# Kernel optimization log

Hardware: AMD Instinct MI355X
Metric: run time of the kernel (lower is better)

Reference implementation:

```python
import jax, jax.numpy as jnp
import numpy as np

B, S, D, E, H = 8, 1024, 1024, 8, 4096  # batch, seq, n_embd, num_experts, 4*n_embd


def setup_inputs() -> dict:
    key = jax.random.key(0)
    ks = jax.random.split(key, 8)
    sc = 0.02
    return {
        "x": jax.random.normal(ks[0], (B, S, D), jnp.float32),
        "noise": jax.random.normal(ks[1], (B, S, E), jnp.float32),
        "Wg": jax.random.normal(ks[2], (D, E), jnp.float32) * sc,
        "bg": jnp.zeros((E,), jnp.float32),
        "Wn": jax.random.normal(ks[3], (D, E), jnp.float32) * sc,
        "bn": jnp.zeros((E,), jnp.float32),
        "W1": jax.random.normal(ks[4], (E, D, H), jnp.float32) * sc,
        "b1": jnp.zeros((E, H), jnp.float32),
        "W2": jax.random.normal(ks[5], (E, H, D), jnp.float32) * sc,
        "b2": jnp.zeros((E, D), jnp.float32),
        "top_k": 2,
    }


def reference(x, noise, Wg, bg, Wn, bn, W1, b1, W2, b2, top_k):
    # --- NoisyTopkRouter ---
    logits = jnp.einsum("bsd,de->bse", x, Wg) + bg
    noise_logits = jnp.einsum("bsd,de->bse", x, Wn) + bn
    noisy = logits + noise * jax.nn.softplus(noise_logits)  # [B,S,E]
    _, idx = jax.lax.top_k(noisy, top_k)  # [B,S,K]
    in_topk = jax.nn.one_hot(idx, noisy.shape[-1], dtype=noisy.dtype).sum(-2) > 0
    sparse_logits = jnp.where(in_topk, noisy, -jnp.inf)
    gating = jax.nn.softmax(sparse_logits, axis=-1)  # zero outside top-k

    # --- dispatch/combine: gating is exactly zero for non-selected experts,
    # so per-expert masked gather + weighted scatter-add == gated dense sum ---
    g_e = jnp.moveaxis(gating, -1, 0)  # [E,B,S]

    def body(acc, params):
        W1e, b1e, W2e, b2e, ge = params
        h = jax.nn.relu(jnp.einsum("bsd,dh->bsh", x, W1e) + b1e)  # [B,S,H]
        y = (jnp.einsum("bsh,hd->bsd", h, W2e) + b2e) * ge[..., None]
        return acc + y, y

    final_output, expert_outputs = jax.lax.scan(
        body, jnp.zeros_like(x), (W1, b1, W2, b2, g_e)
    )
    # expert_outputs: [E,B,S,D], matching the per-expert weighted outputs list
    return final_output, expert_outputs, gating
```

## Files before the change

kernel.cpp:

```cpp
#include <hip/hip_runtime.h>
#include <hip/hip_bf16.h>
#include <stdint.h>

#define TKN   8192
#define DD    1024
#define EE    8
#define HH    4096
#define TOPK  2
#define NASG  (TKN * TOPK)
#define NSLOT 72

typedef unsigned short u16;
typedef __bf16 bf16x8 __attribute__((ext_vector_type(8)));
typedef float  f32x4  __attribute__((ext_vector_type(4)));

__device__ __forceinline__ u16 f2bf(float f) {
  __hip_bfloat16 h = __float2bfloat16(f);
  return __builtin_bit_cast(u16, h);
}
__device__ __forceinline__ float bf2f(u16 u) {
  uint32_t v = ((uint32_t)u) << 16;
  return __builtin_bit_cast(float, v);
}

__device__ __forceinline__ void glds16(const void* g, void* l) {
  __builtin_amdgcn_global_load_lds(
      (__attribute__((address_space(1))) void*)g,
      (__attribute__((address_space(3))) void*)l, 16, 0, 0);
}

#define FENCE() asm volatile("" ::: "memory")
#define BAR()   do { FENCE(); __builtin_amdgcn_s_barrier(); FENCE(); } while (0)
#define VMCNT8() asm volatile("s_waitcnt vmcnt(8)" ::: "memory")
#define VMCNT0() asm volatile("s_waitcnt vmcnt(0)" ::: "memory")

__global__ __launch_bounds__(256) void transpose_cvt_kernel(
    const float* __restrict__ src, u16* __restrict__ dst, int R, int C) {
  __shared__ float tile[64][33];
  int e = blockIdx.z;
  int c0 = blockIdx.x * 32, r0 = blockIdx.y * 64;
  int tx = threadIdx.x, ty = threadIdx.y;
  const float* s = src + (size_t)e * R * C;
  uint32_t* d32 = (uint32_t*)(dst + (size_t)e * R * C);
#pragma unroll
  for (int j = 0; j < 8; j++)
    tile[ty * 8 + j][tx] = s[(size_t)(r0 + ty * 8 + j) * C + c0 + tx];
  __syncthreads();
#pragma unroll
  for (int jj = 0; jj < 4; jj++) {
    int c = c0 + ty * 4 + jj;
    uint32_t lo = f2bf(tile[2 * tx][ty * 4 + jj]);
    uint32_t hi = f2bf(tile[2 * tx + 1][ty * 4 + jj]);
    d32[((size_t)c * R + r0) / 2 + tx] = lo | (hi << 16);
  }
}

__global__ __launch_bounds__(256) void router_kernel(
    const float* __restrict__ x, const float* __restrict__ noise,
    const float* __restrict__ Wg, const float* __restrict__ bg,
    const float* __restrict__ Wn, const float* __restrict__ bn,
    float* __restrict__ gating, u16* __restrict__ xb,
    int* __restrict__ sel_e, float* __restrict__ sel_g) {
  int t = blockIdx.x;
  int tid = threadIdx.x;
  float acc[16];
#pragma unroll
  for (int j = 0; j < 16; j++) acc[j] = 0.f;
  for (int i = tid; i < DD; i += 256) {
    float xv = x[(size_t)t * DD + i];
    xb[(size_t)t * DD + i] = f2bf(xv);
    const float4* g4 = (const float4*)(Wg + (size_t)i * EE);
    const float4* n4 = (const float4*)(Wn + (size_t)i * EE);
    float4 ga = g4[0], gb = g4[1];
    float4 na = n4[0], nb = n4[1];
    acc[0] += xv * ga.x;  acc[1] += xv * ga.y;  acc[2] += xv * ga.z;  acc[3] += xv * ga.w;
    acc[4] += xv * gb.x;  acc[5] += xv * gb.y;  acc[6] += xv * gb.z;  acc[7] += xv * gb.w;
    acc[8] += xv * na.x;  acc[9] += xv * na.y;  acc[10] += xv * na.z; acc[11] += xv * na.w;
    acc[12] += xv * nb.x; acc[13] += xv * nb.y; acc[14] += xv * nb.z; acc[15] += xv * nb.w;
  }
  __shared__ float red[4][16];
  int lane = tid & 63, wv = tid >> 6;
#pragma unroll
  for (int j = 0; j < 16; j++) {
    float v = acc[j];
    for (int o = 32; o > 0; o >>= 1) v += __shfl_down(v, o);
    acc[j] = v;
  }
  if (lane == 0) {
#pragma unroll
    for (int j = 0; j < 16; j++) red[wv][j] = acc[j];
  }
  __syncthreads();
  if (tid == 0) {
    float nz[EE];
#pragma unroll
    for (int e = 0; e < EE; e++) {
      float dg = red[0][e] + red[1][e] + red[2][e] + red[3][e] + bg[e];
      float dn = red[0][8 + e] + red[1][8 + e] + red[2][8 + e] + red[3][8 + e] + bn[e];
      float sp = fmaxf(dn, 0.f) + log1pf(expf(-fabsf(dn)));
      nz[e] = dg + noise[(size_t)t * EE + e] * sp;
    }
    int m1 = 0;
    for (int e = 1; e < EE; e++) if (nz[e] > nz[m1]) m1 = e;
    int m2 = (m1 == 0) ? 1 : 0;
    for (int e = 0; e < EE; e++) if (e != m1 && nz[e] > nz[m2]) m2 = e;
    float eb = expf(nz[m2] - nz[m1]);
    float den = 1.f + eb;
    float g1 = 1.f / den, g2 = eb / den;
    gating[(size_t)t * EE + m1] = g1;
    gating[(size_t)t * EE + m2] = g2;
    sel_e[t * 2] = m1; sel_e[t * 2 + 1] = m2;
    sel_g[t * 2] = g1; sel_g[t * 2 + 1] = g2;
  }
}

__global__ __launch_bounds__(256) void hist_scan_kernel(
    const int* __restrict__ sel_e, int* __restrict__ counts,
    int* __restrict__ offsets, int* __restrict__ cursors,
    int* __restrict__ slots) {
  __shared__ int hist[EE];
  int tid = threadIdx.x;
  if (tid < EE) hist[tid] = 0;
  __syncthreads();
  for (int i = tid; i < NASG; i += 256) atomicAdd(&hist[sel_e[i]], 1);
  __syncthreads();
  if (tid == 0) {
    int off = 0, ns = 0;
    for (int e = 0; e < EE; e++) {
      int c = hist[e];
      counts[e] = c; offsets[e] = off; cursors[e] = off; off += c;
      int nrt = (c + 255) >> 8;
      for (int rt = 0; rt < nrt; rt++) slots[ns++] = (e << 16) | rt;
    }
    for (; ns < NSLOT; ns++) slots[ns] = -1;
  }
}

__global__ __launch_bounds__(256) void build_lists_kernel(
    const int* __restrict__ sel_e, const float* __restrict__ sel_g,
    int* __restrict__ cursors, int* __restrict__ tok_list,
    float* __restrict__ gate_list, int* __restrict__ asg_of) {
  int t = blockIdx.x * 256 + threadIdx.x;
  int lane = threadIdx.x & 63;
#pragma unroll
  for (int k = 0; k < TOPK; k++) {
    int e = sel_e[t * 2 + k];
    float g = sel_g[t * 2 + k];
    for (int ee = 0; ee < EE; ee++) {
      unsigned long long m = __ballot(e == ee);
      if (m) {
        int leader = __ffsll(m) - 1;
        int base = 0;
        if (lane == leader) base = atomicAdd(&cursors[ee], __popcll(m));
        base = __shfl(base, leader);
        if (e == ee) {
          int slot = base + __popcll(m & ((1ull << lane) - 1ull));
          tok_list[slot] = t;
          gate_list[slot] = g;
          asg_of[t * 2 + k] = slot;
        }
      }
    }
  }
}

__global__ __launch_bounds__(256) void zerofill_kernel(
    const float* __restrict__ gating, float* __restrict__ expert_out) {
  int id = blockIdx.x;
  int e = id >> 13, t = id & (TKN - 1);
  if (gating[(size_t)t * EE + e] != 0.f) return;
  float4* p = (float4*)(expert_out + ((size_t)e * TKN + t) * DD);
  p[threadIdx.x] = (float4){0.f, 0.f, 0.f, 0.f};
}

__global__ __launch_bounds__(256) void combine_kernel(
    const float* __restrict__ expert_out, const int* __restrict__ sel_e,
    float* __restrict__ final_out) {
  int t = blockIdx.x;
  int e1 = sel_e[2 * t], e2 = sel_e[2 * t + 1];
  const float4* r1 = (const float4*)(expert_out + ((size_t)e1 * TKN + t) * DD);
  const float4* r2 = (const float4*)(expert_out + ((size_t)e2 * TKN + t) * DD);
  float4* o = (float4*)(final_out + (size_t)t * DD);
  int i = threadIdx.x;
  float4 a = r1[i], b = r2[i];
  o[i] = (float4){a.x + b.x, a.y + b.y, a.z + b.z, a.w + b.w};
}

__global__ __launch_bounds__(256) void merge_combine_kernel(
    const u16* __restrict__ part, const int* __restrict__ asg_of,
    const int* __restrict__ sel_e, const float* __restrict__ sel_g,
    const float* __restrict__ b2, float* __restrict__ expert_out,
    float* __restrict__ final_out) {
  int t = blockIdx.x;
  int i = threadIdx.x;
  int i1 = asg_of[2 * t], i2 = asg_of[2 * t + 1];
  int e1 = sel_e[2 * t], e2 = sel_e[2 * t + 1];
  float g1 = sel_g[2 * t], g2 = sel_g[2 * t + 1];
  float s1[4] = {0.f, 0.f, 0.f, 0.f}, s2[4] = {0.f, 0.f, 0.f, 0.f};
#pragma unroll
  for (int kq = 0; kq < 4; kq++) {
    ushort4 a = ((const ushort4*)(part + ((size_t)kq * NASG + i1) * DD))[i];
    ushort4 b = ((const ushort4*)(part + ((size_t)kq * NASG + i2) * DD))[i];
    s1[0] += bf2f(a.x); s1[1] += bf2f(a.y); s1[2] += bf2f(a.z); s1[3] += bf2f(a.w);
    s2[0] += bf2f(b.x); s2[1] += bf2f(b.y); s2[2] += bf2f(b.z); s2[3] += bf2f(b.w);
  }
  float4 bb1 = ((const float4*)(b2 + (size_t)e1 * DD))[i];
  float4 bb2 = ((const float4*)(b2 + (size_t)e2 * DD))[i];
  float4 y1 = {(s1[0] + bb1.x) * g1, (s1[1] + bb1.y) * g1,
               (s1[2] + bb1.z) * g1, (s1[3] + bb1.w) * g1};
  float4 y2 = {(s2[0] + bb2.x) * g2, (s2[1] + bb2.y) * g2,
               (s2[2] + bb2.z) * g2, (s2[3] + bb2.w) * g2};
  ((float4*)(expert_out + ((size_t)e1 * TKN + t) * DD))[i] = y1;
  ((float4*)(expert_out + ((size_t)e2 * TKN + t) * DD))[i] = y2;
  ((float4*)(final_out + (size_t)t * DD))[i] =
      (float4){y1.x + y2.x, y1.y + y2.y, y1.z + y2.z, y1.w + y2.w};
}

template<int KLOOP, int KSTRIDE, bool GATHER, int EPI, int LOGC>
__global__ __launch_bounds__(512, 2) void gemm8_kernel(
    const u16* __restrict__ A, const u16* __restrict__ Bm,
    const float* __restrict__ bias, const int* __restrict__ tok_list,
    const float* __restrict__ gate_list, const int* __restrict__ counts,
    const int* __restrict__ offsets, const int* __restrict__ slots,
    int Ncols, u16* __restrict__ OutBf, float* __restrict__ outF,
    u16* __restrict__ outP) {
  constexpr int NT = KLOOP / 64;
  int gid = blockIdx.x;
  int q = gid >> 3;
  constexpr int PERX = 9 << LOGC;
  int kq = q / PERX;
  int r0q = q - kq * PERX;
  int slot = (gid & 7) * 9 + (r0q >> LOGC);
  int ct = r0q & ((1 << LOGC) - 1);
  int packed = slots[slot];
  if (packed < 0) return;
  int e = packed >> 16;
  int rt = packed & 0xffff;
  int cnt = counts[e];
  int off = offsets[e];
  int col0 = ct * 256;
  int k0e = kq * KLOOP;

  __shared__ __attribute__((aligned(16))) char ldsc[131072];

  int tid = threadIdx.x;
  int w = tid >> 6, l = tid & 63;
  int wm = w >> 2, wn = w & 3;
  int fr = l & 15, hi = l >> 4;
  int kk16 = hi << 4;
  int xr = (fr & 7) << 4;

  int rl0 = w * 8 + (l >> 3);
  int slotE = ((l & 7) ^ ((l >> 3) & 7)) << 3;
  const u16* aptr[4];
  const u16* bptr[4];
#pragma unroll
  for (int i = 0; i < 4; i++) {
    int r = rt * 256 + rl0 + i * 64;
    if (GATHER) {
      int idx = min(off + r, NASG - 1);
      aptr[i] = A + (size_t)tok_list[idx] * KSTRIDE + k0e + slotE;
    } else {
      aptr[i] = A + (size_t)(off + r) * KSTRIDE + k0e + slotE;
    }
    bptr[i] = Bm + ((size_t)e * Ncols + col0 + rl0 + i * 64) * KSTRIDE + k0e + slotE;
  }
  char* ldsA = ldsc;
  char* ldsB = ldsc + 65536;

  auto issueA = [&](int t, int h) {
    char* d = ldsA + (t & 1) * 32768 + h * 16384 + w * 1024;
    glds16(aptr[h * 2 + 0] + t * 64, d);
    glds16(aptr[h * 2 + 1] + t * 64, d + 8192);
  };
  auto issueB = [&](int t, int h) {
    char* d = ldsB + (t & 1) * 32768 + h * 16384 + w * 1024;
    glds16(bptr[h * 2 + 0] + t * 64, d);
    glds16(bptr[h * 2 + 1] + t * 64, d + 8192);
  };

  f32x4 acc[8][4];
#pragma unroll
  for (int m = 0; m < 8; m++)
#pragma unroll
    for (int n = 0; n < 4; n++) acc[m][n] = (f32x4){0.f, 0.f, 0.f, 0.f};
  bf16x8 aF[4][2], bF0[2][2], bF1[2][2];

  issueB(0, 0); issueB(0, 1); issueA(0, 0); issueA(0, 1);
  issueB(1, 0); issueB(1, 1); issueA(1, 0); issueA(1, 1);
  VMCNT8();
  BAR();

  for (int t = 0; t < NT; t++) {
    int abase = (t & 1) * 32768;
    int bbase = 65536 + (t & 1) * 32768;
#pragma unroll
    for (int mm = 0; mm < 4; mm++)
#pragma unroll
      for (int ks = 0; ks < 2; ks++)
        aF[mm][ks] = *(const bf16x8*)(ldsc + abase + (wm * 128 + mm * 16 + fr) * 128 +
                                      ((ks * 64 + kk16) ^ xr));
#pragma unroll
    for (int nn = 0; nn < 2; nn++)
#pragma unroll
      for (int ks = 0; ks < 2; ks++)
        bF0[nn][ks] = *(const bf16x8*)(ldsc + bbase + (wn * 64 + nn * 16 + fr) * 128 +
                                       ((ks * 64 + kk16) ^ xr));
    BAR();
    __builtin_amdgcn_s_setprio(1);
#pragma unroll
    for (int mm = 0; mm < 4; mm++)
#pragma unroll
      for (int nn = 0; nn < 2; nn++)
#pragma unroll
        for (int ks = 0; ks < 2; ks++)
          acc[mm][nn] = __builtin_amdgcn_mfma_f32_16x16x32_bf16(aF[mm][ks], bF0[nn][ks], acc[mm][nn], 0, 0, 0);
    __builtin_amdgcn_s_setprio(0);
    BAR();
#pragma unroll
    for (int nn = 0; nn < 2; nn++)
#pragma unroll
      for (int ks = 0; ks < 2; ks++)
        bF1[nn][ks] = *(const bf16x8*)(ldsc + bbase + (wn * 64 + 32 + nn * 16 + fr) * 128 +
                                       ((ks * 64 + kk16) ^ xr));
    BAR();
    __builtin_amdgcn_s_setprio(1);
#pragma unroll
    for (int mm = 0; mm < 4; mm++)
#pragma unroll
      for (int nn = 0; nn < 2; nn++)
#pragma unroll
        for (int ks = 0; ks < 2; ks++)
          acc[mm][2 + nn] = __builtin_amdgcn_mfma_f32_16x16x32_bf16(aF[mm][ks], bF1[nn][ks], acc[mm][2 + nn], 0, 0, 0);
    __builtin_amdgcn_s_setprio(0);
    BAR();
#pragma unroll
    for (int mm = 0; mm < 4; mm++)
#pragma unroll
      for (int ks = 0; ks < 2; ks++)
        aF[mm][ks] = *(const bf16x8*)(ldsc + abase + (wm * 128 + 64 + mm * 16 + fr) * 128 +
                                      ((ks * 64 + kk16) ^ xr));
    if (t + 2 < NT) { issueB(t + 2, 0); issueB(t + 2, 1); }
    BAR();
    __builtin_amdgcn_s_setprio(1);
#pragma unroll
    for (int mm = 0; mm < 4; mm++)
#pragma unroll
      for (int nn = 0; nn < 2; nn++)
#pragma unroll
        for (int ks = 0; ks < 2; ks++)
          acc[4 + mm][nn] = __builtin_amdgcn_mfma_f32_16x16x32_bf16(aF[mm][ks], bF0[nn][ks], acc[4 + mm][nn], 0, 0, 0);
    __builtin_amdgcn_s_setprio(0);
    BAR();
    if (t + 2 < NT) {
      issueA(t + 2, 0); issueA(t + 2, 1);
      VMCNT8();
    } else {
      VMCNT0();
    }
    BAR();
    __builtin_amdgcn_s_setprio(1);
#pragma unroll
    for (int mm = 0; mm < 4; mm++)
#pragma unroll
      for (int nn = 0; nn < 2; nn++)
#pragma unroll
        for (int ks = 0; ks < 2; ks++)
          acc[4 + mm][2 + nn] = __builtin_amdgcn_mfma_f32_16x16x32_bf16(aF[mm][ks], bF1[nn][ks], acc[4 + mm][2 + nn], 0, 0, 0);
    __builtin_amdgcn_s_setprio(0);
    BAR();
  }

  float biasN[4];
  int cN[4];
#pragma unroll
  for (int n = 0; n < 4; n++) {
    cN[n] = col0 + wn * 64 + (n >> 1) * 32 + (n & 1) * 16 + fr;
    biasN[n] = (EPI == 2) ? 0.f : bias[e * Ncols + cN[n]];
  }
  if constexpr (EPI == 0) {
#pragma unroll
    for (int m = 0; m < 8; m++) {
      int rb = rt * 256 + wm * 128 + (m >> 2) * 64 + (m & 3) * 16 + hi * 4;
#pragma unroll
      for (int j = 0; j < 4; j++) {
        int r = rb + j;
        if (r < cnt) {
#pragma unroll
          for (int n = 0; n < 4; n++) {
            float v = acc[m][n][j] + biasN[n];
            OutBf[(size_t)(off + r) * Ncols + cN[n]] = f2bf(fmaxf(v, 0.f));
          }
        }
      }
    }
  } else if constexpr (EPI == 1) {
#pragma unroll
    for (int m = 0; m < 8; m++) {
      int rb = rt * 256 + wm * 128 + (m >> 2) * 64 + (m & 3) * 16 + hi * 4;
#pragma unroll
      for (int j = 0; j < 4; j++) {
        int r = rb + j;
        if (r < cnt) {
          int idx = off + r;
          int tok = tok_list[idx];
          float g = gate_list[idx];
          size_t erow = ((size_t)e * TKN + tok) * DD;
#pragma unroll
          for (int n = 0; n < 4; n++)
            outF[erow + cN[n]] = (acc[m][n][j] + biasN[n]) * g;
        }
      }
    }
  } else {
#pragma unroll
    for (int m = 0; m < 8; m++) {
      int rb = rt * 256 + wm * 128 + (m >> 2) * 64 + (m & 3) * 16 + hi * 4;
#pragma unroll
      for (int j = 0; j < 4; j++) {
        int r = rb + j;
        if (r < cnt) {
          size_t prow = ((size_t)kq * NASG + off + r) * DD;
#pragma unroll
          for (int n = 0; n < 4; n++)
            outP[prow + cN[n]] = f2bf(acc[m][n][j]);
        }
      }
    }
  }
}

extern "C" void kernel_launch(void* const* d_in, const int* in_sizes, int n_in,
                              void* d_out, int out_size, void* d_ws, size_t ws_size,
                              hipStream_t stream) {
  const float* x     = (const float*)d_in[0];
  const float* noise = (const float*)d_in[1];
  const float* Wg    = (const float*)d_in[2];
  const float* bg    = (const float*)d_in[3];
  const float* Wn    = (const float*)d_in[4];
  const float* bn    = (const float*)d_in[5];
  const float* W1    = (const float*)d_in[6];
  const float* b1    = (const float*)d_in[7];
  const float* W2    = (const float*)d_in[8];
  const float* b2    = (const float*)d_in[9];

  float* final_out  = (float*)d_out;
  float* expert_out = final_out + (size_t)TKN * DD;
  float* gating     = expert_out + (size_t)EE * TKN * DD;

  char* ws = (char*)d_ws;
  size_t o = 0;
  auto alloc = [&](size_t bytes) {
    char* p = ws + o;
    o += bytes;
    o = (o + 255) & ~(size_t)255;
    return p;
  };
  u16*   xb        = (u16*)alloc((size_t)TKN * DD * 2);
  u16*   w1t       = (u16*)alloc((size_t)EE * HH * DD * 2);
  u16*   w2t       = (u16*)alloc((size_t)EE * DD * HH * 2);
  u16*   hbuf      = (u16*)alloc(((size_t)NASG + 256) * HH * 2);
  int*   tok_list  = (int*)alloc((size_t)NASG * 4);
  float* gate_list = (float*)alloc((size_t)NASG * 4);
  int*   sel_e     = (int*)alloc((size_t)NASG * 4);
  float* sel_g     = (float*)alloc((size_t)NASG * 4);
  int*   asg_of    = (int*)alloc((size_t)NASG * 4);
  int*   counts    = (int*)alloc(256);
  int*   offsets   = (int*)alloc(256);
  int*   cursors   = (int*)alloc(256);
  int*   slots     = (int*)alloc(NSLOT * 4);
  u16*   part      = (u16*)alloc((size_t)4 * NASG * DD * 2);
  bool use_split = (o <= ws_size);

  hipMemsetAsync(gating, 0, (size_t)TKN * EE * sizeof(float), stream);

  router_kernel<<<TKN, 256, 0, stream>>>(x, noise, Wg, bg, Wn, bn, gating, xb, sel_e, sel_g);
  hist_scan_kernel<<<1, 256, 0, stream>>>(sel_e, counts, offsets, cursors, slots);
  build_lists_kernel<<<TKN / 256, 256, 0, stream>>>(sel_e, sel_g, cursors, tok_list,
                                                    gate_list, asg_of);
  zerofill_kernel<<<EE * TKN, 256, 0, stream>>>(gating, expert_out);

  transpose_cvt_kernel<<<dim3(HH / 32, DD / 64, EE), dim3(32, 8), 0, stream>>>(W1, w1t, DD, HH);
  transpose_cvt_kernel<<<dim3(DD / 32, HH / 64, EE), dim3(32, 8), 0, stream>>>(W2, w2t, HH, DD);

  gemm8_kernel<DD, DD, true, 0, 4><<<8 * 9 * 16, 512, 0, stream>>>(
      xb, w1t, b1, tok_list, nullptr, counts, offsets, slots, HH, hbuf, nullptr, nullptr);

  if (use_split) {
    gemm8_kernel<HH / 4, HH, false, 2, 2><<<8 * 9 * 4 * 4, 512, 0, stream>>>(
        hbuf, w2t, b2, tok_list, gate_list, counts, offsets, slots, DD, nullptr, nullptr, part);
    merge_combine_kernel<<<TKN, 256, 0, stream>>>(part, asg_of, sel_e, sel_g, b2,
                                                  expert_out, final_out);
  } else {
    gemm8_kernel<HH, HH, false, 1, 2><<<8 * 9 * 4, 512, 0, stream>>>(
        hbuf, w2t, b2, tok_list, gate_list, counts, offsets, slots, DD, nullptr, expert_out, nullptr);
    combine_kernel<<<TKN, 256, 0, stream>>>(expert_out, sel_e, final_out);
  }
}
```

Before: 629.4 us.

## Simplify GEMM main loop to single-barrier double buffering with prefetch distance one

Replaces the multi-phase main loop, which had eight barriers per K-tile and split A/B prefetches issued two tiles ahead, with one merged A+B prefetch of the next tile at the start of each iteration. The four MFMA quadrants are merged into two blocks, and the loop ends with a single vmcnt(0) wait and barrier. The goal is to cut barrier and synchronisation overhead. The cost is that each load now gets only one tile of compute to hide its global-to-LDS latency, and the interleaving between waves from the staggered barriers is lost.

```diff
diff --git a/kernel.cpp b/kernel.cpp
--- a/kernel.cpp
+++ b/kernel.cpp
@@ -31,7 +31,6 @@
 
 #define FENCE() asm volatile("" ::: "memory")
 #define BAR()   do { FENCE(); __builtin_amdgcn_s_barrier(); FENCE(); } while (0)
-#define VMCNT8() asm volatile("s_waitcnt vmcnt(8)" ::: "memory")
 #define VMCNT0() asm volatile("s_waitcnt vmcnt(0)" ::: "memory")
 
 __global__ __launch_bounds__(256) void transpose_cvt_kernel(
@@ -268,15 +267,17 @@
   char* ldsA = ldsc;
   char* ldsB = ldsc + 65536;
 
-  auto issueA = [&](int t, int h) {
-    char* d = ldsA + (t & 1) * 32768 + h * 16384 + w * 1024;
-    glds16(aptr[h * 2 + 0] + t * 64, d);
-    glds16(aptr[h * 2 + 1] + t * 64, d + 8192);
-  };
-  auto issueB = [&](int t, int h) {
-    char* d = ldsB + (t & 1) * 32768 + h * 16384 + w * 1024;
-    glds16(bptr[h * 2 + 0] + t * 64, d);
-    glds16(bptr[h * 2 + 1] + t * 64, d + 8192);
+  auto issueAB = [&](int t) {
+    char* db = ldsB + (t & 1) * 32768 + w * 1024;
+    char* da = ldsA + (t & 1) * 32768 + w * 1024;
+    glds16(bptr[0] + t * 64, db);
+    glds16(bptr[1] + t * 64, db + 8192);
+    glds16(bptr[2] + t * 64, db + 16384);
+    glds16(bptr[3] + t * 64, db + 24576);
+    glds16(aptr[0] + t * 64, da);
+    glds16(aptr[1] + t * 64, da + 8192);
+    glds16(aptr[2] + t * 64, da + 16384);
+    glds16(aptr[3] + t * 64, da + 24576);
   };
 
   f32x4 acc[8][4];
@@ -286,14 +287,14 @@
     for (int n = 0; n < 4; n++) acc[m][n] = (f32x4){0.f, 0.f, 0.f, 0.f};
   bf16x8 aF[4][2], bF0[2][2], bF1[2][2];
 
-  issueB(0, 0); issueB(0, 1); issueA(0, 0); issueA(0, 1);
-  issueB(1, 0); issueB(1, 1); issueA(1, 0); issueA(1, 1);
-  VMCNT8();
+  issueAB(0);
+  VMCNT0();
   BAR();
 
   for (int t = 0; t < NT; t++) {
     int abase = (t & 1) * 32768;
     int bbase = 65536 + (t & 1) * 32768;
+    if (t + 1 < NT) issueAB(t + 1);
 #pragma unroll
     for (int mm = 0; mm < 4; mm++)
 #pragma unroll
@@ -303,71 +304,41 @@
 #pragma unroll
     for (int nn = 0; nn < 2; nn++)
 #pragma unroll
-      for (int ks = 0; ks < 2; ks++)
+      for (int ks = 0; ks < 2; ks++) {
         bF0[nn][ks] = *(const bf16x8*)(ldsc + bbase + (wn * 64 + nn * 16 + fr) * 128 +
                                        ((ks * 64 + kk16) ^ xr));
-    BAR();
-    __builtin_amdgcn_s_setprio(1);
-#pragma unroll
-    for (int mm = 0; mm < 4; mm++)
-#pragma unroll
-      for (int nn = 0; nn < 2; nn++)
-#pragma unroll
-        for (int ks = 0; ks < 2; ks++)
-          acc[mm][nn] = __builtin_amdgcn_mfma_f32_16x16x32_bf16(aF[mm][ks], bF0[nn][ks], acc[mm][nn], 0, 0, 0);
-    __builtin_amdgcn_s_setprio(0);
-    BAR();
-#pragma unroll
-    for (int nn = 0; nn < 2; nn++)
-#pragma unroll
-      for (int ks = 0; ks < 2; ks++)
         bF1[nn][ks] = *(const bf16x8*)(ldsc + bbase + (wn * 64 + 32 + nn * 16 + fr) * 128 +
                                        ((ks * 64 + kk16) ^ xr));
-    BAR();
+      }
     __builtin_amdgcn_s_setprio(1);
 #pragma unroll
     for (int mm = 0; mm < 4; mm++)
 #pragma unroll
       for (int nn = 0; nn < 2; nn++)
 #pragma unroll
-        for (int ks = 0; ks < 2; ks++)
+        for (int ks = 0; ks < 2; ks++) {
+          acc[mm][nn]     = __builtin_amdgcn_mfma_f32_16x16x32_bf16(aF[mm][ks], bF0[nn][ks], acc[mm][nn], 0, 0, 0);
           acc[mm][2 + nn] = __builtin_amdgcn_mfma_f32_16x16x32_bf16(aF[mm][ks], bF1[nn][ks], acc[mm][2 + nn], 0, 0, 0);
+        }
     __builtin_amdgcn_s_setprio(0);
-    BAR();
 #pragma unroll
     for (int mm = 0; mm < 4; mm++)
 #pragma unroll
       for (int ks = 0; ks < 2; ks++)
         aF[mm][ks] = *(const bf16x8*)(ldsc + abase + (wm * 128 + 64 + mm * 16 + fr) * 128 +
                                       ((ks * 64 + kk16) ^ xr));
-    if (t + 2 < NT) { issueB(t + 2, 0); issueB(t + 2, 1); }
-    BAR();
     __builtin_amdgcn_s_setprio(1);
 #pragma unroll
     for (int mm = 0; mm < 4; mm++)
 #pragma unroll
       for (int nn = 0; nn < 2; nn++)
 #pragma unroll
-        for (int ks = 0; ks < 2; ks++)
-          acc[4 + mm][nn] = __builtin_amdgcn_mfma_f32_16x16x32_bf16(aF[mm][ks], bF0[nn][ks], acc[4 + mm][nn], 0, 0, 0);
+        for (int ks = 0; ks < 2; ks++) {
+          acc[4 + mm][nn]     = __builtin_amdgcn_mfma_f32_16x16x32_bf16(aF[mm][ks], bF0[nn][ks], acc[4 + mm][nn], 0, 0, 0);
+          acc[4 + mm][2 + nn] = __builtin_amdgcn_mfma_f32_16x16x32_bf16(aF[mm][ks], bF1[nn][ks], acc[4 + mm][2 + nn], 0, 0, 0);
+        }
     __builtin_amdgcn_s_setprio(0);
-    BAR();
-    if (t + 2 < NT) {
-      issueA(t + 2, 0); issueA(t + 2, 1);
-      VMCNT8();
-    } else {
-      VMCNT0();
-    }
-    BAR();
-    __builtin_amdgcn_s_setprio(1);
-#pragma unroll
-    for (int mm = 0; mm < 4; mm++)
-#pragma unroll
-      for (int nn = 0; nn < 2; nn++)
-#pragma unroll
-        for (int ks = 0; ks < 2; ks++)
-          acc[4 + mm][2 + nn] = __builtin_amdgcn_mfma_f32_16x16x32_bf16(aF[mm][ks], bF1[nn][ks], acc[4 + mm][2 + nn], 0, 0, 0);
-    __builtin_amdgcn_s_setprio(0);
+    VMCNT0();
     BAR();
   }
 
```

After: 611.1 us. 1.03x faster.
